# Kernel optimization log

Hardware: AMD Instinct MI355X
Metric: run time of the kernel (lower is better)

The kernel has to match this reference:

```python
import jax, jax.numpy as jnp
import numpy as np

N_EMBD = 1024  # C in forward; scale is C**-0.5 (full embed dim, per source)


def setup_inputs() -> dict:
    key = jax.random.key(0)
    k1, k2, k3, k4 = jax.random.split(key, 4)
    B, T, C, H = 4, 4096, N_EMBD, 64
    x = jax.random.normal(k1, (B, T, C), dtype=jnp.float32)
    # weights stored as [in, out] = [n_embd, head_size]
    Wq = jax.random.normal(k2, (C, H), dtype=jnp.float32) * (C ** -0.5)
    Wk = jax.random.normal(k3, (C, H), dtype=jnp.float32) * (C ** -0.5)
    Wv = jax.random.normal(k4, (C, H), dtype=jnp.float32) * (C ** -0.5)
    return {"x": x, "Wq": Wq, "Wk": Wk, "Wv": Wv}


def reference(x, Wq, Wk, Wv):
    # x: [B, T, C]; projections to head_size H
    C = x.shape[-1]
    q = jnp.einsum('btc,ch->bth', x, Wq)  # [B,T,H]
    k = jnp.einsum('btc,ch->bth', x, Wk)  # [B,T,H]
    v = jnp.einsum('btc,ch->bth', x, Wv)  # [B,T,H]
    # scores scaled by C**-0.5 (full embed dim, matching original module)
    wei = jnp.einsum('bth,bsh->bts', q, k) * (C ** -0.5)  # [B,T,T]
    wei = jax.nn.softmax(wei, axis=-1)  # dropout p=0 -> identity
    out = jnp.einsum('bts,bsh->bth', wei, v)  # [B,T,H]
    return out
```

## Files before the change

kernel.cpp:

```cpp
#include <hip/hip_runtime.h>
#include <hip/hip_bf16.h>


#define BB 4
#define TT 4096
#define CC 1024
#define HH 64

typedef __attribute__((ext_vector_type(8))) short bf16x8;
typedef __attribute__((ext_vector_type(4))) float f32x4;

__device__ __forceinline__ short f2bf(float f) {
  union { float f; unsigned u; } v; v.f = f;
  unsigned r = v.u + 0x7fffu + ((v.u >> 16) & 1u);
  return (short)(r >> 16);
}

__global__ void wtf_kernel(const float* __restrict__ Wq, const float* __restrict__ Wk,
                           const float* __restrict__ Wv, short* __restrict__ WtF) {
  int idx = blockIdx.x * 256 + threadIdx.x;
  int lane = idx & 63, ks = (idx >> 6) & 31, nf = idx >> 11;
  int l15 = lane & 15, lg = lane >> 4;
  int n = nf * 16 + l15;
  const float* W = (n < HH) ? Wq : ((n < 2 * HH) ? Wk : Wv);
  float sc = (n < HH) ? 0.03125f : 1.0f;
  int k0 = ks * 32 + lg * 8, h = n & (HH - 1);
  bf16x8 r;
#pragma unroll
  for (int j = 0; j < 8; ++j) r[j] = f2bf(W[(k0 + j) * HH + h] * sc);
  *(bf16x8*)(WtF + (size_t)idx * 8) = r;
}

__launch_bounds__(256, 4)
__global__ void proj_kernel(const float* __restrict__ x, const short* __restrict__ WtF,
                            short* __restrict__ qo, short* __restrict__ ko,
                            short* __restrict__ vTo) {
  __shared__ __align__(16) short xs[16 * 1024];
  int t = threadIdx.x;
  int row0 = blockIdx.x * 16;

  {
    int r = t >> 4, kc = t & 15;
    const float4* xr4 = (const float4*)(x + (size_t)(row0 + r) * CC) + kc * 2;
#pragma unroll
    for (int i = 0; i < 8; ++i) {
      float4 a = xr4[i * 32], b2 = xr4[i * 32 + 1];
      bf16x8 w;
      w[0] = f2bf(a.x);  w[1] = f2bf(a.y);  w[2] = f2bf(a.z);  w[3] = f2bf(a.w);
      w[4] = f2bf(b2.x); w[5] = f2bf(b2.y); w[6] = f2bf(b2.z); w[7] = f2bf(b2.w);
      int c = kc + i * 16;
      int S = (c * 256 + r * 16) ^ ((c & 7) << 4);
      *(bf16x8*)((char*)xs + S) = w;
    }
  }
  __syncthreads();

  int wave = t >> 6, lane = t & 63;
  int l15 = lane & 15, lg = lane >> 4;
  int nf0 = wave * 3;
  const short* wp = WtF + ((size_t)nf0 * 32 * 64 + (size_t)lane) * 8;
  const char* xsb = (const char*)xs;

  f32x4 acc[3];
#pragma unroll
  for (int j = 0; j < 3; ++j) acc[j] = (f32x4){0.f, 0.f, 0.f, 0.f};

  bf16x8 wA[3], wB[3];
#pragma unroll
  for (int j = 0; j < 3; ++j) wA[j] = *(const bf16x8*)(wp + (size_t)j * 32 * 512);

#pragma unroll
  for (int ks = 0; ks < 32; ks += 2) {
#pragma unroll
    for (int j = 0; j < 3; ++j)
      wB[j] = *(const bf16x8*)(wp + ((size_t)j * 32 + ks + 1) * 512);
    bf16x8 a0 = *(const bf16x8*)(xsb + ks * 1024 +
                   ((lane * 16) ^ ((((ks * 4) + lg) & 7) << 4)));
#pragma unroll
    for (int j = 0; j < 3; ++j)
      acc[j] = __builtin_amdgcn_mfma_f32_16x16x32_bf16(a0, wA[j], acc[j], 0, 0, 0);
    if (ks + 2 < 32) {
#pragma unroll
      for (int j = 0; j < 3; ++j)
        wA[j] = *(const bf16x8*)(wp + ((size_t)j * 32 + ks + 2) * 512);
    }
    bf16x8 a1 = *(const bf16x8*)(xsb + (ks + 1) * 1024 +
                   ((lane * 16) ^ (((((ks + 1) * 4) + lg) & 7) << 4)));
#pragma unroll
    for (int j = 0; j < 3; ++j)
      acc[j] = __builtin_amdgcn_mfma_f32_16x16x32_bf16(a1, wB[j], acc[j], 0, 0, 0);
  }

#pragma unroll
  for (int j = 0; j < 3; ++j) {
    int nf = nf0 + j;
    int h = (nf & 3) * 16 + l15;
    if (nf < 8) {
      short* dst = (nf < 4) ? qo : ko;
#pragma unroll
      for (int reg = 0; reg < 4; ++reg)
        dst[(size_t)(row0 + lg * 4 + reg) * HH + h] = f2bf(acc[j][reg]);
    } else {
      int b = row0 >> 12;
      int trow = (row0 & 4095) + lg * 4;
      short4 s4;
      s4.x = f2bf(acc[j][0]); s4.y = f2bf(acc[j][1]);
      s4.z = f2bf(acc[j][2]); s4.w = f2bf(acc[j][3]);
      *(short4*)(vTo + ((size_t)b * HH + h) * TT + trow) = s4;
    }
  }
}

__global__ void kperm_kernel(const short* __restrict__ k, short* __restrict__ kF) {
  int idx = blockIdx.x * 256 + threadIdx.x;
  int lane = idx & 63, ld = (idx >> 6) & 7, kt = (idx >> 9) & 63, b = idx >> 15;
  int l15 = lane & 15, lg = lane >> 4;
  int kpos = kt * 64 + (ld >> 1) * 16 + l15;
  int e0 = (ld & 1) * 32 + lg * 8;
  bf16x8 r = *(const bf16x8*)(k + ((size_t)b * TT + kpos) * HH + e0);
  *(bf16x8*)(kF + (size_t)idx * 8) = r;
}

__global__ void vperm_kernel(const short* __restrict__ vT, short* __restrict__ vF) {
  int idx = blockIdx.x * 256 + threadIdx.x;
  int lane = idx & 63, ld = (idx >> 6) & 7, kt = (idx >> 9) & 63, b = idx >> 15;
  int l15 = lane & 15, lg = lane >> 4;
  int h = (ld >> 1) * 16 + l15;
  int spos = kt * 64 + (ld & 1) * 32 + lg * 8;
  bf16x8 r = *(const bf16x8*)(vT + ((size_t)b * HH + h) * TT + spos);
  *(bf16x8*)(vF + (size_t)idx * 8) = r;
}

__launch_bounds__(512, 2)
__global__ void attnF_kernel(const short* __restrict__ q, const short* __restrict__ kF,
                             const short* __restrict__ vF, float* __restrict__ out) {
  __shared__ __align__(16) short ps[8][16 * 64];
  __shared__ __align__(16) float macc[4][16 * 68];
  __shared__ float ml[4][16];
  int wave = threadIdx.x >> 6, lane = threadIdx.x & 63;
  int l15 = lane & 15, lg = lane >> 4;
  int qtile = wave & 3, half = wave >> 2;
  int low3 = blockIdx.x & 7;
  int b  = low3 >> 1;
  int qt = ((blockIdx.x >> 3) << 1) | (low3 & 1);
  int row0 = qt * 64 + qtile * 16;

  const short* qb = q + ((size_t)b * TT + row0 + l15) * HH;
  bf16x8 qa0 = *(const bf16x8*)(qb + lg * 8);
  bf16x8 qa1 = *(const bf16x8*)(qb + 32 + lg * 8);
  const short* kfb = kF + (size_t)b * (64 * 8 * 64 * 8) + (size_t)lane * 8;
  const short* vfb = vF + (size_t)b * (64 * 8 * 64 * 8) + (size_t)lane * 8;

  f32x4 acc[4];
#pragma unroll
  for (int i = 0; i < 4; ++i) acc[i] = (f32x4){0.f, 0.f, 0.f, 0.f};
  float lsum[4] = {0.f, 0.f, 0.f, 0.f};

  char* psw = (char*)&ps[wave][0];
  int lgs = lg * 512;
  int lgm = (lg & 1) << 6;
  int mreg[4], col2[4];
#pragma unroll
  for (int reg = 0; reg < 4; ++reg) mreg[reg] = lgm | (reg << 4);
#pragma unroll
  for (int cf = 0; cf < 4; ++cf) col2[cf] = l15 * 2 + cf * 32;
  int rofs0 = (l15 * 128 + 0 + lg * 16) ^ ((l15 & 7) << 4);
  int rofs1 = (l15 * 128 + 64 + lg * 16) ^ ((l15 & 7) << 4);

  int kt0 = half * 32, ktN = kt0 + 32;

  for (int kt = kt0; kt < ktN; ++kt) {
    const short* kp = kfb + (size_t)kt * 4096;
    const short* vp = vfb + (size_t)kt * 4096;
    bf16x8 kf[8], vf[8];
#pragma unroll
    for (int ld = 0; ld < 8; ++ld) kf[ld] = *(const bf16x8*)(kp + ld * 512);
#pragma unroll
    for (int ld = 0; ld < 8; ++ld) vf[ld] = *(const bf16x8*)(vp + ld * 512);
#pragma unroll
    for (int cf = 0; cf < 4; ++cf) {
      f32x4 tt = (f32x4){0.f, 0.f, 0.f, 0.f};
      tt = __builtin_amdgcn_mfma_f32_16x16x32_bf16(qa0, kf[cf * 2], tt, 0, 0, 0);
      tt = __builtin_amdgcn_mfma_f32_16x16x32_bf16(qa1, kf[cf * 2 + 1], tt, 0, 0, 0);
#pragma unroll
      for (int reg = 0; reg < 4; ++reg) {
        float p = __expf(tt[reg]);
        lsum[reg] += p;
        *(short*)(psw + ((col2[cf] ^ mreg[reg]) + lgs + reg * 128)) = f2bf(p);
      }
    }
    bf16x8 pa0 = *(const bf16x8*)(psw + rofs0);
    bf16x8 pa1 = *(const bf16x8*)(psw + rofs1);
    __builtin_amdgcn_s_setprio(1);
#pragma unroll
    for (int hf = 0; hf < 4; ++hf) {
      acc[hf] = __builtin_amdgcn_mfma_f32_16x16x32_bf16(pa0, vf[hf * 2], acc[hf], 0, 0, 0);
      acc[hf] = __builtin_amdgcn_mfma_f32_16x16x32_bf16(pa1, vf[hf * 2 + 1], acc[hf], 0, 0, 0);
    }
    __builtin_amdgcn_s_setprio(0);
  }

#pragma unroll
  for (int reg = 0; reg < 4; ++reg) {
    float r = lsum[reg];
    r += __shfl_xor(r, 1); r += __shfl_xor(r, 2);
    r += __shfl_xor(r, 4); r += __shfl_xor(r, 8);
    lsum[reg] = r;
  }

  if (half) {
#pragma unroll
    for (int reg = 0; reg < 4; ++reg) {
      int row = lg * 4 + reg;
#pragma unroll
      for (int hf = 0; hf < 4; ++hf)
        macc[qtile][row * 68 + hf * 16 + l15] = acc[hf][reg];
      if (l15 == 0) ml[qtile][row] = lsum[reg];
    }
  }
  __syncthreads();
  if (!half) {
#pragma unroll
    for (int reg = 0; reg < 4; ++reg) {
      int row = lg * 4 + reg;
      float inv = 1.0f / (lsum[reg] + ml[qtile][row]);
#pragma unroll
      for (int hf = 0; hf < 4; ++hf) {
        float o = acc[hf][reg] + macc[qtile][row * 68 + hf * 16 + l15];
        out[((size_t)b * TT + row0 + row) * HH + hf * 16 + l15] = o * inv;
      }
    }
  }
}

extern "C" void kernel_launch(void* const* d_in, const int* in_sizes, int n_in,
                              void* d_out, int out_size, void* d_ws, size_t ws_size,
                              hipStream_t stream) {
  const float* x  = (const float*)d_in[0];
  const float* Wq = (const float*)d_in[1];
  const float* Wk = (const float*)d_in[2];
  const float* Wv = (const float*)d_in[3];
  float* out = (float*)d_out;

  char* ws = (char*)d_ws;
  short* WtF = (short*)ws;
  short* q   = (short*)(ws + 0x080000);
  short* k   = (short*)(ws + 0x280000);
  short* vT  = (short*)(ws + 0x480000);
  short* kF  = (short*)(ws + 0x680000);
  short* vF  = (short*)(ws + 0x880000);

  hipLaunchKernelGGL(wtf_kernel,  dim3(96),   dim3(256), 0, stream, Wq, Wk, Wv, WtF);
  hipLaunchKernelGGL(proj_kernel, dim3(1024), dim3(256), 0, stream, x, WtF, q, k, vT);
  hipLaunchKernelGGL(kperm_kernel, dim3(512), dim3(256), 0, stream, k, kF);
  hipLaunchKernelGGL(vperm_kernel, dim3(512), dim3(256), 0, stream, vT, vF);
  hipLaunchKernelGGL(attnF_kernel, dim3(256), dim3(512), 0, stream, q, kF, vF, out);
}
```

Measured before the change: 74.41 us.

## Give each attention wave 32 query rows over a quarter of keys

The attention kernel is reorganised so each wave handles two 16-row query groups (32 rows) across one quarter of the key range, instead of 16 rows across half the keys. Each loaded K/V fragment is now reused by two query groups, which halves global loads per MFMA. The four key-quarter partials are merged through shared memory in phased syncs, and the output is written with vectorised float4 stores. Separately, log2(e) is folded into the Q weight scale so the kernel can use exp2f instead of __expf. The costs are higher register use for two accumulator sets and extra barriers in the reduction.

```diff
diff --git a/kernel.cpp b/kernel.cpp
--- a/kernel.cpp
+++ b/kernel.cpp
@@ -23,7 +23,7 @@
   int l15 = lane & 15, lg = lane >> 4;
   int n = nf * 16 + l15;
   const float* W = (n < HH) ? Wq : ((n < 2 * HH) ? Wk : Wv);
-  float sc = (n < HH) ? 0.03125f : 1.0f;
+  float sc = (n < HH) ? (0.03125f * 1.44269504f) : 1.0f;
   int k0 = ks * 32 + lg * 8, h = n & (HH - 1);
   bf16x8 r;
 #pragma unroll
@@ -132,104 +132,121 @@
 }
 
 __launch_bounds__(512, 2)
-__global__ void attnF_kernel(const short* __restrict__ q, const short* __restrict__ kF,
+__global__ void attnQ_kernel(const short* __restrict__ q, const short* __restrict__ kF,
                              const short* __restrict__ vF, float* __restrict__ out) {
-  __shared__ __align__(16) short ps[8][16 * 64];
-  __shared__ __align__(16) float macc[4][16 * 68];
-  __shared__ float ml[4][16];
+  __shared__ __align__(16) short ps[8][1280];
+  __shared__ __align__(16) float macc[64][68];
+  __shared__ float lL[64];
   int wave = threadIdx.x >> 6, lane = threadIdx.x & 63;
   int l15 = lane & 15, lg = lane >> 4;
-  int qtile = wave & 3, half = wave >> 2;
+  int qg = wave & 1, qr = wave >> 1;
   int low3 = blockIdx.x & 7;
   int b  = low3 >> 1;
   int qt = ((blockIdx.x >> 3) << 1) | (low3 & 1);
-  int row0 = qt * 64 + qtile * 16;
-
-  const short* qb = q + ((size_t)b * TT + row0 + l15) * HH;
-  bf16x8 qa0 = *(const bf16x8*)(qb + lg * 8);
-  bf16x8 qa1 = *(const bf16x8*)(qb + 32 + lg * 8);
+  int brow0 = qt * 64;
+  int rowW = brow0 + qg * 32;
+
+  const short* qb = q + ((size_t)b * TT + rowW + l15) * HH;
+  bf16x8 qa[2][2];
+  qa[0][0] = *(const bf16x8*)(qb + lg * 8);
+  qa[0][1] = *(const bf16x8*)(qb + 32 + lg * 8);
+  qa[1][0] = *(const bf16x8*)(qb + 16 * HH + lg * 8);
+  qa[1][1] = *(const bf16x8*)(qb + 16 * HH + 32 + lg * 8);
+
   const short* kfb = kF + (size_t)b * (64 * 8 * 64 * 8) + (size_t)lane * 8;
   const short* vfb = vF + (size_t)b * (64 * 8 * 64 * 8) + (size_t)lane * 8;
 
-  f32x4 acc[4];
-#pragma unroll
-  for (int i = 0; i < 4; ++i) acc[i] = (f32x4){0.f, 0.f, 0.f, 0.f};
-  float lsum[4] = {0.f, 0.f, 0.f, 0.f};
+  f32x4 acc[2][4];
+#pragma unroll
+  for (int g = 0; g < 2; ++g)
+#pragma unroll
+    for (int i = 0; i < 4; ++i) acc[g][i] = (f32x4){0.f, 0.f, 0.f, 0.f};
+  float lsum[2][4] = {{0.f, 0.f, 0.f, 0.f}, {0.f, 0.f, 0.f, 0.f}};
 
   char* psw = (char*)&ps[wave][0];
-  int lgs = lg * 512;
-  int lgm = (lg & 1) << 6;
-  int mreg[4], col2[4];
-#pragma unroll
-  for (int reg = 0; reg < 4; ++reg) mreg[reg] = lgm | (reg << 4);
-#pragma unroll
-  for (int cf = 0; cf < 4; ++cf) col2[cf] = l15 * 2 + cf * 32;
-  int rofs0 = (l15 * 128 + 0 + lg * 16) ^ ((l15 & 7) << 4);
-  int rofs1 = (l15 * 128 + 64 + lg * 16) ^ ((l15 & 7) << 4);
-
-  int kt0 = half * 32, ktN = kt0 + 32;
-
-  for (int kt = kt0; kt < ktN; ++kt) {
-    const short* kp = kfb + (size_t)kt * 4096;
-    const short* vp = vfb + (size_t)kt * 4096;
-    bf16x8 kf[8], vf[8];
-#pragma unroll
-    for (int ld = 0; ld < 8; ++ld) kf[ld] = *(const bf16x8*)(kp + ld * 512);
-#pragma unroll
-    for (int ld = 0; ld < 8; ++ld) vf[ld] = *(const bf16x8*)(vp + ld * 512);
-#pragma unroll
-    for (int cf = 0; cf < 4; ++cf) {
-      f32x4 tt = (f32x4){0.f, 0.f, 0.f, 0.f};
-      tt = __builtin_amdgcn_mfma_f32_16x16x32_bf16(qa0, kf[cf * 2], tt, 0, 0, 0);
-      tt = __builtin_amdgcn_mfma_f32_16x16x32_bf16(qa1, kf[cf * 2 + 1], tt, 0, 0, 0);
-#pragma unroll
-      for (int reg = 0; reg < 4; ++reg) {
-        float p = __expf(tt[reg]);
-        lsum[reg] += p;
-        *(short*)(psw + ((col2[cf] ^ mreg[reg]) + lgs + reg * 128)) = f2bf(p);
+  int pw = lg * 4 * 80 + ((l15 * 2) ^ ((lg >> 1) << 4));
+  int pr = l15 * 80 + ((lg ^ (l15 >> 3)) << 4);
+
+  for (int t = qr * 32; t < qr * 32 + 32; ++t) {
+    const short* kp = kfb + (size_t)t * 2048;
+    const short* vp = vfb + (size_t)(t >> 1) * 4096 + (size_t)(t & 1) * 512;
+    bf16x8 kf[4], vf[4];
+#pragma unroll
+    for (int ld = 0; ld < 4; ++ld) kf[ld] = *(const bf16x8*)(kp + ld * 512);
+#pragma unroll
+    for (int hf = 0; hf < 4; ++hf) vf[hf] = *(const bf16x8*)(vp + hf * 1024);
+#pragma unroll
+    for (int g = 0; g < 2; ++g)
+#pragma unroll
+      for (int cf = 0; cf < 2; ++cf) {
+        f32x4 t4 = (f32x4){0.f, 0.f, 0.f, 0.f};
+        t4 = __builtin_amdgcn_mfma_f32_16x16x32_bf16(qa[g][0], kf[cf * 2], t4, 0, 0, 0);
+        t4 = __builtin_amdgcn_mfma_f32_16x16x32_bf16(qa[g][1], kf[cf * 2 + 1], t4, 0, 0, 0);
+#pragma unroll
+        for (int reg = 0; reg < 4; ++reg) {
+          float p = exp2f(t4[reg]);
+          lsum[g][reg] += p;
+          *(short*)(psw + (g * 1280 + pw + reg * 80 + cf * 32)) = f2bf(p);
+        }
       }
-    }
-    bf16x8 pa0 = *(const bf16x8*)(psw + rofs0);
-    bf16x8 pa1 = *(const bf16x8*)(psw + rofs1);
+    bf16x8 pa0 = *(const bf16x8*)(psw + pr);
+    bf16x8 pa1 = *(const bf16x8*)(psw + 1280 + pr);
     __builtin_amdgcn_s_setprio(1);
 #pragma unroll
     for (int hf = 0; hf < 4; ++hf) {
-      acc[hf] = __builtin_amdgcn_mfma_f32_16x16x32_bf16(pa0, vf[hf * 2], acc[hf], 0, 0, 0);
-      acc[hf] = __builtin_amdgcn_mfma_f32_16x16x32_bf16(pa1, vf[hf * 2 + 1], acc[hf], 0, 0, 0);
+      acc[0][hf] = __builtin_amdgcn_mfma_f32_16x16x32_bf16(pa0, vf[hf], acc[0][hf], 0, 0, 0);
+      acc[1][hf] = __builtin_amdgcn_mfma_f32_16x16x32_bf16(pa1, vf[hf], acc[1][hf], 0, 0, 0);
     }
     __builtin_amdgcn_s_setprio(0);
   }
 
 #pragma unroll
-  for (int reg = 0; reg < 4; ++reg) {
-    float r = lsum[reg];
-    r += __shfl_xor(r, 1); r += __shfl_xor(r, 2);
-    r += __shfl_xor(r, 4); r += __shfl_xor(r, 8);
-    lsum[reg] = r;
-  }
-
-  if (half) {
+  for (int g = 0; g < 2; ++g)
 #pragma unroll
     for (int reg = 0; reg < 4; ++reg) {
-      int row = lg * 4 + reg;
-#pragma unroll
-      for (int hf = 0; hf < 4; ++hf)
-        macc[qtile][row * 68 + hf * 16 + l15] = acc[hf][reg];
-      if (l15 == 0) ml[qtile][row] = lsum[reg];
-    }
-  }
-  __syncthreads();
-  if (!half) {
-#pragma unroll
-    for (int reg = 0; reg < 4; ++reg) {
-      int row = lg * 4 + reg;
-      float inv = 1.0f / (lsum[reg] + ml[qtile][row]);
-#pragma unroll
-      for (int hf = 0; hf < 4; ++hf) {
-        float o = acc[hf][reg] + macc[qtile][row * 68 + hf * 16 + l15];
-        out[((size_t)b * TT + row0 + row) * HH + hf * 16 + l15] = o * inv;
+      float r = lsum[g][reg];
+      r += __shfl_xor(r, 1); r += __shfl_xor(r, 2);
+      r += __shfl_xor(r, 4); r += __shfl_xor(r, 8);
+      lsum[g][reg] = r;
+    }
+
+#pragma unroll
+  for (int ph = 0; ph < 4; ++ph) {
+    if (qr == ph) {
+#pragma unroll
+      for (int g = 0; g < 2; ++g) {
+#pragma unroll
+        for (int reg = 0; reg < 4; ++reg) {
+          int row = qg * 32 + g * 16 + lg * 4 + reg;
+          if (ph == 0) {
+#pragma unroll
+            for (int hf = 0; hf < 4; ++hf)
+              macc[row][hf * 16 + l15] = acc[g][hf][reg];
+            if (l15 == 0) lL[row] = lsum[g][reg];
+          } else {
+#pragma unroll
+            for (int hf = 0; hf < 4; ++hf)
+              macc[row][hf * 16 + l15] += acc[g][hf][reg];
+            if (l15 == 0) lL[row] += lsum[g][reg];
+          }
+        }
       }
     }
+    __syncthreads();
+  }
+
+  {
+    int t = threadIdx.x;
+    int r = t >> 3, c0 = (t & 7) * 8;
+    float linv = 1.0f / lL[r];
+    float4 o0, o1;
+    o0.x = macc[r][c0 + 0] * linv; o0.y = macc[r][c0 + 1] * linv;
+    o0.z = macc[r][c0 + 2] * linv; o0.w = macc[r][c0 + 3] * linv;
+    o1.x = macc[r][c0 + 4] * linv; o1.y = macc[r][c0 + 5] * linv;
+    o1.z = macc[r][c0 + 6] * linv; o1.w = macc[r][c0 + 7] * linv;
+    float* op = out + ((size_t)b * TT + brow0 + r) * HH + c0;
+    *(float4*)op = o0;
+    *(float4*)(op + 4) = o1;
   }
 }
 
@@ -250,9 +267,9 @@
   short* kF  = (short*)(ws + 0x680000);
   short* vF  = (short*)(ws + 0x880000);
 
-  hipLaunchKernelGGL(wtf_kernel,  dim3(96),   dim3(256), 0, stream, Wq, Wk, Wv, WtF);
-  hipLaunchKernelGGL(proj_kernel, dim3(1024), dim3(256), 0, stream, x, WtF, q, k, vT);
-  hipLaunchKernelGGL(kperm_kernel, dim3(512), dim3(256), 0, stream, k, kF);
-  hipLaunchKernelGGL(vperm_kernel, dim3(512), dim3(256), 0, stream, vT, vF);
-  hipLaunchKernelGGL(attnF_kernel, dim3(256), dim3(512), 0, stream, q, kF, vF, out);
-}
+  hipLaunchKernelGGL(wtf_kernel,   dim3(96),   dim3(256), 0, stream, Wq, Wk, Wv, WtF);
+  hipLaunchKernelGGL(proj_kernel,  dim3(1024), dim3(256), 0, stream, x, WtF, q, k, vT);
+  hipLaunchKernelGGL(kperm_kernel, dim3(512),  dim3(256), 0, stream, k, kF);
+  hipLaunchKernelGGL(vperm_kernel, dim3(512),  dim3(256), 0, stream, vT, vF);
+  hipLaunchKernelGGL(attnQ_kernel, dim3(256),  dim3(512), 0, stream, q, kF, vF, out);
+}
```

New measurement: 76.28 us. 2.5% more time.

## Stage K/V tiles through double-buffered LDS with direct global-to-LDS loads

Applied to the files above, without the earlier changes.

The attention kernel now loads each K/V tile cooperatively into a double-buffered shared-memory area using global_load_lds. Every wave fetches one slice per tile, so each block reads K and V once instead of once per wave, and the next tile is prefetched while the current one is computed. The key-range split between the two wave halves is now interleaved within each tile rather than split into two contiguous ranges. The log2(e) factor is folded into the Wq scale so exp2f can replace __expf, and the hardware bf16 conversion replaces the manual rounding. This adds a block-wide barrier every iteration and more LDS use, which may lower occupancy.

```diff
diff --git a/kernel.cpp b/kernel.cpp
--- a/kernel.cpp
+++ b/kernel.cpp
@@ -16,6 +16,17 @@
   return (short)(r >> 16);
 }
 
+__device__ __forceinline__ short f2bf_hw(float f) {
+  __hip_bfloat16 h = __float2bfloat16(f);
+  return *reinterpret_cast<short*>(&h);
+}
+
+__device__ __forceinline__ void gload16(const short* g, short* l) {
+  __builtin_amdgcn_global_load_lds(
+      (const __attribute__((address_space(1))) void*)g,
+      (__attribute__((address_space(3))) void*)l, 16, 0, 0);
+}
+
 __global__ void wtf_kernel(const float* __restrict__ Wq, const float* __restrict__ Wk,
                            const float* __restrict__ Wv, short* __restrict__ WtF) {
   int idx = blockIdx.x * 256 + threadIdx.x;
@@ -23,7 +34,7 @@
   int l15 = lane & 15, lg = lane >> 4;
   int n = nf * 16 + l15;
   const float* W = (n < HH) ? Wq : ((n < 2 * HH) ? Wk : Wv);
-  float sc = (n < HH) ? 0.03125f : 1.0f;
+  float sc = (n < HH) ? (0.03125f * 1.44269504f) : 1.0f;
   int k0 = ks * 32 + lg * 8, h = n & (HH - 1);
   bf16x8 r;
 #pragma unroll
@@ -131,10 +142,11 @@
   *(bf16x8*)(vF + (size_t)idx * 8) = r;
 }
 
-__launch_bounds__(512, 2)
-__global__ void attnF_kernel(const short* __restrict__ q, const short* __restrict__ kF,
+__launch_bounds__(512)
+__global__ void attnL_kernel(const short* __restrict__ q, const short* __restrict__ kF,
                              const short* __restrict__ vF, float* __restrict__ out) {
-  __shared__ __align__(16) short ps[8][16 * 64];
+  __shared__ __align__(16) short kvs[2 * 2 * 4096];
+  __shared__ __align__(16) short ps[8][640];
   __shared__ __align__(16) float macc[4][16 * 68];
   __shared__ float ml[4][16];
   int wave = threadIdx.x >> 6, lane = threadIdx.x & 63;
@@ -148,8 +160,13 @@
   const short* qb = q + ((size_t)b * TT + row0 + l15) * HH;
   bf16x8 qa0 = *(const bf16x8*)(qb + lg * 8);
   bf16x8 qa1 = *(const bf16x8*)(qb + 32 + lg * 8);
-  const short* kfb = kF + (size_t)b * (64 * 8 * 64 * 8) + (size_t)lane * 8;
-  const short* vfb = vF + (size_t)b * (64 * 8 * 64 * 8) + (size_t)lane * 8;
+
+  const short* kfb = kF + (size_t)b * 262144;
+  const short* vfb = vF + (size_t)b * 262144;
+
+  int cbase = (wave & 3) * 2;
+  int isV = half;
+  short* ldsS = kvs + isV * 4096 + cbase * 512;
 
   f32x4 acc[4];
 #pragma unroll
@@ -157,47 +174,51 @@
   float lsum[4] = {0.f, 0.f, 0.f, 0.f};
 
   char* psw = (char*)&ps[wave][0];
-  int lgs = lg * 512;
-  int lgm = (lg & 1) << 6;
-  int mreg[4], col2[4];
-#pragma unroll
-  for (int reg = 0; reg < 4; ++reg) mreg[reg] = lgm | (reg << 4);
-#pragma unroll
-  for (int cf = 0; cf < 4; ++cf) col2[cf] = l15 * 2 + cf * 32;
-  int rofs0 = (l15 * 128 + 0 + lg * 16) ^ ((l15 & 7) << 4);
-  int rofs1 = (l15 * 128 + 64 + lg * 16) ^ ((l15 & 7) << 4);
-
-  int kt0 = half * 32, ktN = kt0 + 32;
-
-  for (int kt = kt0; kt < ktN; ++kt) {
-    const short* kp = kfb + (size_t)kt * 4096;
-    const short* vp = vfb + (size_t)kt * 4096;
-    bf16x8 kf[8], vf[8];
-#pragma unroll
-    for (int ld = 0; ld < 8; ++ld) kf[ld] = *(const bf16x8*)(kp + ld * 512);
-#pragma unroll
-    for (int ld = 0; ld < 8; ++ld) vf[ld] = *(const bf16x8*)(vp + ld * 512);
-#pragma unroll
-    for (int cf = 0; cf < 4; ++cf) {
-      f32x4 tt = (f32x4){0.f, 0.f, 0.f, 0.f};
-      tt = __builtin_amdgcn_mfma_f32_16x16x32_bf16(qa0, kf[cf * 2], tt, 0, 0, 0);
-      tt = __builtin_amdgcn_mfma_f32_16x16x32_bf16(qa1, kf[cf * 2 + 1], tt, 0, 0, 0);
+  int pw = lg * 320 + ((l15 * 2) ^ ((lg >> 1) << 4));
+  int pr = l15 * 80 + ((lg ^ (l15 >> 3)) << 4);
+
+  {
+    const short* src = (isV ? vfb : kfb) + cbase * 512 + lane * 8;
+    gload16(src, ldsS);
+    gload16(src + 512, ldsS + 512);
+  }
+  __syncthreads();
+
+  int cur = 0;
+  for (int t = 0; t < 64; ++t) {
+    if (t < 63) {
+      const short* src = (isV ? vfb : kfb) + (size_t)(t + 1) * 4096 + cbase * 512 + lane * 8;
+      short* dst = ldsS + (cur ^ 1) * 8192;
+      gload16(src, dst);
+      gload16(src + 512, dst + 512);
+    }
+    const short* ldsK = kvs + cur * 8192 + (4 * half) * 512;
+    const short* ldsV = kvs + cur * 8192 + 4096 + half * 512;
+    bf16x8 kf[4], vf[4];
+#pragma unroll
+    for (int j = 0; j < 4; ++j) kf[j] = *(const bf16x8*)(ldsK + j * 512 + lane * 8);
+#pragma unroll
+    for (int hf = 0; hf < 4; ++hf) vf[hf] = *(const bf16x8*)(ldsV + hf * 1024 + lane * 8);
+#pragma unroll
+    for (int cf = 0; cf < 2; ++cf) {
+      f32x4 t4 = (f32x4){0.f, 0.f, 0.f, 0.f};
+      t4 = __builtin_amdgcn_mfma_f32_16x16x32_bf16(qa0, kf[cf * 2], t4, 0, 0, 0);
+      t4 = __builtin_amdgcn_mfma_f32_16x16x32_bf16(qa1, kf[cf * 2 + 1], t4, 0, 0, 0);
 #pragma unroll
       for (int reg = 0; reg < 4; ++reg) {
-        float p = __expf(tt[reg]);
+        float p = exp2f(t4[reg]);
         lsum[reg] += p;
-        *(short*)(psw + ((col2[cf] ^ mreg[reg]) + lgs + reg * 128)) = f2bf(p);
+        *(short*)(psw + (pw + reg * 80 + cf * 32)) = f2bf_hw(p);
       }
     }
-    bf16x8 pa0 = *(const bf16x8*)(psw + rofs0);
-    bf16x8 pa1 = *(const bf16x8*)(psw + rofs1);
+    bf16x8 pa = *(const bf16x8*)(psw + pr);
     __builtin_amdgcn_s_setprio(1);
 #pragma unroll
-    for (int hf = 0; hf < 4; ++hf) {
-      acc[hf] = __builtin_amdgcn_mfma_f32_16x16x32_bf16(pa0, vf[hf * 2], acc[hf], 0, 0, 0);
-      acc[hf] = __builtin_amdgcn_mfma_f32_16x16x32_bf16(pa1, vf[hf * 2 + 1], acc[hf], 0, 0, 0);
-    }
+    for (int hf = 0; hf < 4; ++hf)
+      acc[hf] = __builtin_amdgcn_mfma_f32_16x16x32_bf16(pa, vf[hf], acc[hf], 0, 0, 0);
     __builtin_amdgcn_s_setprio(0);
+    __syncthreads();
+    cur ^= 1;
   }
 
 #pragma unroll
@@ -250,9 +271,9 @@
   short* kF  = (short*)(ws + 0x680000);
   short* vF  = (short*)(ws + 0x880000);
 
-  hipLaunchKernelGGL(wtf_kernel,  dim3(96),   dim3(256), 0, stream, Wq, Wk, Wv, WtF);
-  hipLaunchKernelGGL(proj_kernel, dim3(1024), dim3(256), 0, stream, x, WtF, q, k, vT);
-  hipLaunchKernelGGL(kperm_kernel, dim3(512), dim3(256), 0, stream, k, kF);
-  hipLaunchKernelGGL(vperm_kernel, dim3(512), dim3(256), 0, stream, vT, vF);
-  hipLaunchKernelGGL(attnF_kernel, dim3(256), dim3(512), 0, stream, q, kF, vF, out);
-}
+  hipLaunchKernelGGL(wtf_kernel,   dim3(96),   dim3(256), 0, stream, Wq, Wk, Wv, WtF);
+  hipLaunchKernelGGL(proj_kernel,  dim3(1024), dim3(256), 0, stream, x, WtF, q, k, vT);
+  hipLaunchKernelGGL(kperm_kernel, dim3(512),  dim3(256), 0, stream, k, kF);
+  hipLaunchKernelGGL(vperm_kernel, dim3(512),  dim3(256), 0, stream, vT, vF);
+  hipLaunchKernelGGL(attnL_kernel, dim3(256),  dim3(512), 0, stream, q, kF, vF, out);
+}
```

Result: slower. 97.28 us (+30.7%).
